# Optimization experiments

Measured on AMD Instinct MI355X. Metric: run time of the kernel, lower is better.

The kernel has to match this reference:

```python
import jax, jax.numpy as jnp
import numpy as np

N_NODES = 50000
N_EDGES = 800000
HIDDEN = 128
UNIFIED = 128


def _sage_conv(x, src, dst, W_l, b_l, W_r, n_nodes):
    # PyG SAGEConv (mean aggr): out = lin_l(mean_{j in N(i)} x_j) + lin_r(x_i)
    msgs = x[src]  # [E, d] gather of source-node features
    agg = jax.ops.segment_sum(msgs, dst, num_segments=n_nodes)  # [N, d]
    cnt = jax.ops.segment_sum(jnp.ones((src.shape[0],), dtype=x.dtype), dst,
                              num_segments=n_nodes)
    agg = agg / jnp.maximum(cnt, 1.0)[:, None]  # mean; isolated nodes -> 0
    return agg @ W_l.T + b_l + x @ W_r.T


def setup_inputs() -> dict:
    key = jax.random.key(0)
    ks = jax.random.split(key, 8)
    s = 1.0 / np.sqrt(HIDDEN)
    x = jax.random.normal(ks[0], (N_NODES, HIDDEN), dtype=jnp.float32)
    edge_index = jax.random.randint(ks[1], (2, N_EDGES), 0, N_NODES, dtype=jnp.int64)
    W1_l = jax.random.normal(ks[2], (HIDDEN, HIDDEN), dtype=jnp.float32) * s
    b1_l = jnp.zeros((HIDDEN,), dtype=jnp.float32)
    W1_r = jax.random.normal(ks[3], (HIDDEN, HIDDEN), dtype=jnp.float32) * s
    W2_l = jax.random.normal(ks[4], (UNIFIED, HIDDEN), dtype=jnp.float32) * s
    b2_l = jnp.zeros((UNIFIED,), dtype=jnp.float32)
    W2_r = jax.random.normal(ks[5], (UNIFIED, HIDDEN), dtype=jnp.float32) * s
    return {"x": x, "edge_index": edge_index,
            "W1_l": W1_l, "b1_l": b1_l, "W1_r": W1_r,
            "W2_l": W2_l, "b2_l": b2_l, "W2_r": W2_r}


def reference(x, edge_index, W1_l, b1_l, W1_r, W2_l, b2_l, W2_r):
    src, dst = edge_index[0], edge_index[1]
    n = x.shape[0]
    h = jax.nn.relu(_sage_conv(x, src, dst, W1_l, b1_l, W1_r, n))
    return _sage_conv(h, src, dst, W2_l, b2_l, W2_r, n)
```

## Files before the change

kernel.cpp:

```cpp
#include <hip/hip_runtime.h>

#define N_NODES 50000
#define HIDDEN 128
#define NBUCK ((N_NODES + 127) >> 7)
#define BCAP 2304

typedef __attribute__((ext_vector_type(8))) short short8;
typedef __attribute__((ext_vector_type(4))) float f32x4;

__device__ __forceinline__ unsigned short f2bf(float f) {
    union { float f; unsigned int u; } a; a.f = f;
    unsigned int u = a.u;
    u += 0x7FFFu + ((u >> 16) & 1u);
    return (unsigned short)(u >> 16);
}
__device__ __forceinline__ float bf2f(unsigned int bits16) {
    union { unsigned int u; float f; } a; a.u = bits16 << 16;
    return a.f;
}

__global__ __launch_bounds__(256) void pack_both(
    const float* __restrict__ W1l, const float* __restrict__ W1r,
    const float* __restrict__ W2l, const float* __restrict__ W2r,
    unsigned short* __restrict__ Wp1, unsigned short* __restrict__ Wp2,
    int* __restrict__ bcur) {
    int tid = blockIdx.x * blockDim.x + threadIdx.x;
    if (tid < NBUCK) bcur[tid] = tid * BCAP;
    const int which = tid >> 15;
    const int t2 = tid & 32767;
    int j = t2 & 7, lane = (t2 >> 3) & 63, nf = (t2 >> 9) & 7, ks = t2 >> 12;
    int k = ks * 32 + ((lane >> 4) * 8) + j;
    int t = nf * 16 + (lane & 15);
    const float* Wl = which ? W2l : W1l;
    const float* Wr = which ? W2r : W1r;
    float v = (k < 128) ? Wl[t * 128 + k] : Wr[t * 128 + (k - 128)];
    (which ? Wp2 : Wp1)[t2] = f2bf(v);
}

__global__ void cast_bf16(const float* __restrict__ x, unsigned short* __restrict__ xb, int n4) {
    int i = blockIdx.x * blockDim.x + threadIdx.x;
    if (i >= n4) return;
    float4 v = reinterpret_cast<const float4*>(x)[i];
    ushort4 o = make_ushort4(f2bf(v.x), f2bf(v.y), f2bf(v.z), f2bf(v.w));
    reinterpret_cast<ushort4*>(xb)[i] = o;
}

#define PCHUNK 4096
__global__ __launch_bounds__(1024) void partition_edges(
    const int* __restrict__ src, const int* __restrict__ dst, int E,
    int* __restrict__ bcur, unsigned int* __restrict__ packed) {
    __shared__ int h[NBUCK];
    __shared__ int base[NBUCK];
    const int tid = threadIdx.x;
    const int c0 = blockIdx.x * PCHUNK;
    for (int i = tid; i < NBUCK; i += 1024) h[i] = 0;
    __syncthreads();

    unsigned int val[4];
    int bk[4];
#pragma unroll
    for (int u = 0; u < 4; ++u) {
        const int e = c0 + u * 1024 + tid;
        if (e < E) {
            const int d = dst[e];
            val[u] = ((unsigned int)d << 16) | (unsigned int)src[e];
            bk[u] = d >> 7;
            atomicAdd(&h[bk[u]], 1);
        } else {
            bk[u] = -1;
        }
    }
    __syncthreads();
    for (int i = tid; i < NBUCK; i += 1024) {
        base[i] = h[i] ? atomicAdd(&bcur[i], h[i]) : 0;
        h[i] = 0;
    }
    __syncthreads();
#pragma unroll
    for (int u = 0; u < 4; ++u) {
        if (bk[u] >= 0) {
            const int pos = base[bk[u]] + atomicAdd(&h[bk[u]], 1);
            packed[pos] = val[u];
        }
    }
}

__global__ __launch_bounds__(256) void build_rows(const unsigned int* __restrict__ packed,
                                                  const int* __restrict__ bcur,
                                                  int* __restrict__ row_start,
                                                  int* __restrict__ row_end,
                                                  unsigned short* __restrict__ ssrc) {
    __shared__ int lh[128];
    __shared__ int lc[128];
    __shared__ int htot;
    const int b = blockIdx.x;
    const int gbase = b * BCAP, gend = bcur[b];
    const int tid = threadIdx.x;
    if (tid < 128) lh[tid] = 0;
    __syncthreads();
    for (int i = gbase + tid; i < gend; i += 256)
        atomicAdd(&lh[(packed[i] >> 16) & 127], 1);
    __syncthreads();
    int v = 0, incl = 0;
    if (tid < 128) {
        const int lane = tid & 63;
        v = lh[tid];
        incl = v;
#pragma unroll
        for (int off = 1; off < 64; off <<= 1) {
            int t = __shfl_up(incl, off);
            if (lane >= off) incl += t;
        }
        if (tid == 63) htot = incl;
    }
    __syncthreads();
    if (tid < 128) {
        const int excl = incl - v + ((tid >= 64) ? htot : 0);
        lc[tid] = gbase + excl;
        const int node = b * 128 + tid;
        if (node < N_NODES) {
            row_start[node] = gbase + excl;
            row_end[node]   = gbase + excl + v;
        }
    }
    __syncthreads();
    for (int i = gbase + tid; i < gend; i += 256) {
        const unsigned int p = packed[i];
        const int pos = atomicAdd(&lc[(p >> 16) & 127], 1);
        ssrc[pos] = (unsigned short)(p & 0xffffu);
    }
}

__global__ __launch_bounds__(256) void aggregate_mean_bf16(
    const unsigned short* __restrict__ featb, const int* __restrict__ row_start,
    const int* __restrict__ row_end, const unsigned short* __restrict__ ssrc,
    unsigned short* __restrict__ aggb) {
    const int node = blockIdx.x * 16 + (threadIdx.x >> 4);
    const int lq = threadIdx.x & 15;
    if (node >= N_NODES) return;
    const int beg = row_start[node], end = row_end[node];
    float acc[4][8];
#pragma unroll
    for (int u = 0; u < 4; ++u)
#pragma unroll
        for (int f = 0; f < 8; ++f) acc[u][f] = 0.f;

    int j = beg;
    for (; j + 3 < end; j += 4) {
#pragma unroll
        for (int u = 0; u < 4; ++u) {
            const int s = ssrc[j + u];
            const short8 v = *reinterpret_cast<const short8*>(&featb[(size_t)s * HIDDEN + 8 * lq]);
#pragma unroll
            for (int f = 0; f < 8; ++f) acc[u][f] += bf2f((unsigned short)v[f]);
        }
    }
    for (; j < end; ++j) {
        const int s = ssrc[j];
        const short8 v = *reinterpret_cast<const short8*>(&featb[(size_t)s * HIDDEN + 8 * lq]);
#pragma unroll
        for (int f = 0; f < 8; ++f) acc[0][f] += bf2f((unsigned short)v[f]);
    }
    const int d = end - beg;
    const float inv = d ? 1.0f / (float)d : 0.0f;
    short8 o;
#pragma unroll
    for (int f = 0; f < 8; ++f)
        o[f] = (short)f2bf((acc[0][f] + acc[1][f] + acc[2][f] + acc[3][f]) * inv);
    *reinterpret_cast<short8*>(&aggb[(size_t)node * HIDDEN + 8 * lq]) = o;
}

template <int WRITE_BF16_RELU>
__global__ __launch_bounds__(256) void mfma_linear(
    const unsigned short* aggb, const unsigned short* xb,
    const unsigned short* __restrict__ Wp, const float* __restrict__ bias,
    unsigned short* out_b, float* out_f) {
    const int lane = threadIdx.x & 63;
    const int wave = threadIdx.x >> 6;
    const int wm = wave >> 1, wn = wave & 1;
    const int rowbase = blockIdx.x * 64 + wm * 32;
    const int colbase = wn * 64;
    const int l15 = lane & 15, l4 = lane >> 4;

    f32x4 acc[2][4];
#pragma unroll
    for (int m = 0; m < 2; ++m)
#pragma unroll
        for (int nf = 0; nf < 4; ++nf) acc[m][nf] = (f32x4){0.f, 0.f, 0.f, 0.f};

#pragma unroll
    for (int ks = 0; ks < 8; ++ks) {
        const unsigned short* Asrc = (ks < 4) ? aggb : xb;
        const int koff = (ks & 3) * 32 + l4 * 8;
        short8 a[2];
#pragma unroll
        for (int m = 0; m < 2; ++m) {
            int row = rowbase + m * 16 + l15;
            if (row >= N_NODES) row = N_NODES - 1;
            a[m] = *reinterpret_cast<const short8*>(&Asrc[(size_t)row * HIDDEN + koff]);
        }
#pragma unroll
        for (int nf = 0; nf < 4; ++nf) {
            const int nfg = (colbase >> 4) + nf;
            short8 b = *reinterpret_cast<const short8*>(&Wp[(((size_t)ks * 8 + nfg) * 64 + lane) * 8]);
            acc[0][nf] = __builtin_amdgcn_mfma_f32_16x16x32_bf16(a[0], b, acc[0][nf], 0, 0, 0);
            acc[1][nf] = __builtin_amdgcn_mfma_f32_16x16x32_bf16(a[1], b, acc[1][nf], 0, 0, 0);
        }
    }

#pragma unroll
    for (int nf = 0; nf < 4; ++nf) {
        const int col = colbase + nf * 16 + l15;
        const float bv = bias[col];
#pragma unroll
        for (int m = 0; m < 2; ++m) {
#pragma unroll
            for (int r = 0; r < 4; ++r) {
                const int row = rowbase + m * 16 + l4 * 4 + r;
                if (row < N_NODES) {
                    float v = acc[m][nf][r] + bv;
                    if (WRITE_BF16_RELU) {
                        v = fmaxf(v, 0.0f);
                        out_b[(size_t)row * HIDDEN + col] = f2bf(v);
                    } else {
                        out_f[(size_t)row * HIDDEN + col] = v;
                    }
                }
            }
        }
    }
}

extern "C" void kernel_launch(void* const* d_in, const int* in_sizes, int n_in,
                              void* d_out, int out_size, void* d_ws, size_t ws_size,
                              hipStream_t stream) {
    const float* x   = (const float*)d_in[0];
    const int*   ei  = (const int*)d_in[1];
    const float* W1l = (const float*)d_in[2];
    const float* b1  = (const float*)d_in[3];
    const float* W1r = (const float*)d_in[4];
    const float* W2l = (const float*)d_in[5];
    const float* b2  = (const float*)d_in[6];
    const float* W2r = (const float*)d_in[7];

    const int E = in_sizes[1] / 2;
    const int* src = ei;
    const int* dst = ei + E;

    int* iws        = (int*)d_ws;
    int* bcur       = iws;
    int* row_start  = iws + 400;
    int* row_end    = iws + 50400;
    unsigned int* packed = (unsigned int*)(iws + 100400);
    unsigned short* ssrc = (unsigned short*)(iws + 100400 + NBUCK * BCAP);
    unsigned short* xb   = ssrc + (size_t)NBUCK * BCAP;
    unsigned short* aggb = xb + (size_t)N_NODES * HIDDEN;
    unsigned short* Wp1  = aggb + (size_t)N_NODES * HIDDEN;
    unsigned short* Wp2  = Wp1 + 256 * HIDDEN;

    pack_both<<<256, 256, 0, stream>>>(W1l, W1r, W2l, W2r, Wp1, Wp2, bcur);
    cast_bf16<<<(N_NODES * HIDDEN / 4 + 255) / 256, 256, 0, stream>>>(x, xb, N_NODES * HIDDEN / 4);

    partition_edges<<<(E + PCHUNK - 1) / PCHUNK, 1024, 0, stream>>>(src, dst, E, bcur, packed);
    build_rows<<<NBUCK, 256, 0, stream>>>(packed, bcur, row_start, row_end, ssrc);

    const int aggGrid = (N_NODES + 15) / 16;
    const int linGrid = (N_NODES + 63) / 64;

    aggregate_mean_bf16<<<aggGrid, 256, 0, stream>>>(xb, row_start, row_end, ssrc, aggb);
    mfma_linear<1><<<linGrid, 256, 0, stream>>>(aggb, xb, Wp1, b1, xb, nullptr);

    aggregate_mean_bf16<<<aggGrid, 256, 0, stream>>>(xb, row_start, row_end, ssrc, aggb);
    mfma_linear<0><<<linGrid, 256, 0, stream>>>(aggb, xb, Wp2, b2, nullptr, (float*)d_out);
}
```

Baseline: 146.0 us.

## Fuse cast into prep kernel, batch gather loads, retune partition and build_rows

```diff
diff --git a/kernel.cpp b/kernel.cpp
--- a/kernel.cpp
+++ b/kernel.cpp
@@ -4,6 +4,7 @@
 #define HIDDEN 128
 #define NBUCK ((N_NODES + 127) >> 7)
 #define BCAP 2304
+#define CAST_BLOCKS 6250
 
 typedef __attribute__((ext_vector_type(8))) short short8;
 typedef __attribute__((ext_vector_type(4))) float f32x4;
@@ -19,12 +20,21 @@
     return a.f;
 }
 
-__global__ __launch_bounds__(256) void pack_both(
+__global__ __launch_bounds__(256) void prep(
+    const float* __restrict__ x, unsigned short* __restrict__ xb,
     const float* __restrict__ W1l, const float* __restrict__ W1r,
     const float* __restrict__ W2l, const float* __restrict__ W2r,
     unsigned short* __restrict__ Wp1, unsigned short* __restrict__ Wp2,
     int* __restrict__ bcur) {
-    int tid = blockIdx.x * blockDim.x + threadIdx.x;
+    const int b = blockIdx.x;
+    if (b < CAST_BLOCKS) {
+        const int i = b * 256 + threadIdx.x;
+        float4 v = reinterpret_cast<const float4*>(x)[i];
+        ushort4 o = make_ushort4(f2bf(v.x), f2bf(v.y), f2bf(v.z), f2bf(v.w));
+        reinterpret_cast<ushort4*>(xb)[i] = o;
+        return;
+    }
+    const int tid = (b - CAST_BLOCKS) * 256 + threadIdx.x;
     if (tid < NBUCK) bcur[tid] = tid * BCAP;
     const int which = tid >> 15;
     const int t2 = tid & 32767;
@@ -37,15 +47,7 @@
     (which ? Wp2 : Wp1)[t2] = f2bf(v);
 }
 
-__global__ void cast_bf16(const float* __restrict__ x, unsigned short* __restrict__ xb, int n4) {
-    int i = blockIdx.x * blockDim.x + threadIdx.x;
-    if (i >= n4) return;
-    float4 v = reinterpret_cast<const float4*>(x)[i];
-    ushort4 o = make_ushort4(f2bf(v.x), f2bf(v.y), f2bf(v.z), f2bf(v.w));
-    reinterpret_cast<ushort4*>(xb)[i] = o;
-}
-
-#define PCHUNK 4096
+#define PCHUNK 2048
 __global__ __launch_bounds__(1024) void partition_edges(
     const int* __restrict__ src, const int* __restrict__ dst, int E,
     int* __restrict__ bcur, unsigned int* __restrict__ packed) {
@@ -56,10 +58,10 @@
     for (int i = tid; i < NBUCK; i += 1024) h[i] = 0;
     __syncthreads();
 
-    unsigned int val[4];
-    int bk[4];
-#pragma unroll
-    for (int u = 0; u < 4; ++u) {
+    unsigned int val[2];
+    int bk[2];
+#pragma unroll
+    for (int u = 0; u < 2; ++u) {
         const int e = c0 + u * 1024 + tid;
         if (e < E) {
             const int d = dst[e];
@@ -77,7 +79,7 @@
     }
     __syncthreads();
 #pragma unroll
-    for (int u = 0; u < 4; ++u) {
+    for (int u = 0; u < 2; ++u) {
         if (bk[u] >= 0) {
             const int pos = base[bk[u]] + atomicAdd(&h[bk[u]], 1);
             packed[pos] = val[u];
@@ -85,7 +87,7 @@
     }
 }
 
-__global__ __launch_bounds__(256) void build_rows(const unsigned int* __restrict__ packed,
+__global__ __launch_bounds__(512) void build_rows(const unsigned int* __restrict__ packed,
                                                   const int* __restrict__ bcur,
                                                   int* __restrict__ row_start,
                                                   int* __restrict__ row_end,
@@ -98,7 +100,7 @@
     const int tid = threadIdx.x;
     if (tid < 128) lh[tid] = 0;
     __syncthreads();
-    for (int i = gbase + tid; i < gend; i += 256)
+    for (int i = gbase + tid; i < gend; i += 512)
         atomicAdd(&lh[(packed[i] >> 16) & 127], 1);
     __syncthreads();
     int v = 0, incl = 0;
@@ -124,7 +126,7 @@
         }
     }
     __syncthreads();
-    for (int i = gbase + tid; i < gend; i += 256) {
+    for (int i = gbase + tid; i < gend; i += 512) {
         const unsigned int p = packed[i];
         const int pos = atomicAdd(&lc[(p >> 16) & 127], 1);
         ssrc[pos] = (unsigned short)(p & 0xffffu);
@@ -139,34 +141,51 @@
     const int lq = threadIdx.x & 15;
     if (node >= N_NODES) return;
     const int beg = row_start[node], end = row_end[node];
-    float acc[4][8];
-#pragma unroll
-    for (int u = 0; u < 4; ++u)
-#pragma unroll
-        for (int f = 0; f < 8; ++f) acc[u][f] = 0.f;
+    float acc0[8], acc1[8];
+#pragma unroll
+    for (int f = 0; f < 8; ++f) { acc0[f] = 0.f; acc1[f] = 0.f; }
 
     int j = beg;
-    for (; j + 3 < end; j += 4) {
+    for (; j + 7 < end; j += 8) {
+        short8 v[8];
+#pragma unroll
+        for (int u = 0; u < 8; ++u) {
+            const int s = ssrc[j + u];
+            v[u] = *reinterpret_cast<const short8*>(&featb[(size_t)s * HIDDEN + 8 * lq]);
+        }
+#pragma unroll
+        for (int u = 0; u < 8; ++u) {
+            float* a = (u & 1) ? acc1 : acc0;
+#pragma unroll
+            for (int f = 0; f < 8; ++f) a[f] += bf2f((unsigned short)v[u][f]);
+        }
+    }
+    if (j + 3 < end) {
+        short8 v[4];
 #pragma unroll
         for (int u = 0; u < 4; ++u) {
             const int s = ssrc[j + u];
-            const short8 v = *reinterpret_cast<const short8*>(&featb[(size_t)s * HIDDEN + 8 * lq]);
-#pragma unroll
-            for (int f = 0; f < 8; ++f) acc[u][f] += bf2f((unsigned short)v[f]);
-        }
+            v[u] = *reinterpret_cast<const short8*>(&featb[(size_t)s * HIDDEN + 8 * lq]);
+        }
+#pragma unroll
+        for (int u = 0; u < 4; ++u) {
+            float* a = (u & 1) ? acc1 : acc0;
+#pragma unroll
+            for (int f = 0; f < 8; ++f) a[f] += bf2f((unsigned short)v[u][f]);
+        }
+        j += 4;
     }
     for (; j < end; ++j) {
         const int s = ssrc[j];
         const short8 v = *reinterpret_cast<const short8*>(&featb[(size_t)s * HIDDEN + 8 * lq]);
 #pragma unroll
-        for (int f = 0; f < 8; ++f) acc[0][f] += bf2f((unsigned short)v[f]);
+        for (int f = 0; f < 8; ++f) acc0[f] += bf2f((unsigned short)v[f]);
     }
     const int d = end - beg;
     const float inv = d ? 1.0f / (float)d : 0.0f;
     short8 o;
 #pragma unroll
-    for (int f = 0; f < 8; ++f)
-        o[f] = (short)f2bf((acc[0][f] + acc[1][f] + acc[2][f] + acc[3][f]) * inv);
+    for (int f = 0; f < 8; ++f) o[f] = (short)f2bf((acc0[f] + acc1[f]) * inv);
     *reinterpret_cast<short8*>(&aggb[(size_t)node * HIDDEN + 8 * lq]) = o;
 }
 
@@ -258,11 +277,10 @@
     unsigned short* Wp1  = aggb + (size_t)N_NODES * HIDDEN;
     unsigned short* Wp2  = Wp1 + 256 * HIDDEN;
 
-    pack_both<<<256, 256, 0, stream>>>(W1l, W1r, W2l, W2r, Wp1, Wp2, bcur);
-    cast_bf16<<<(N_NODES * HIDDEN / 4 + 255) / 256, 256, 0, stream>>>(x, xb, N_NODES * HIDDEN / 4);
+    prep<<<CAST_BLOCKS + 256, 256, 0, stream>>>(x, xb, W1l, W1r, W2l, W2r, Wp1, Wp2, bcur);
 
     partition_edges<<<(E + PCHUNK - 1) / PCHUNK, 1024, 0, stream>>>(src, dst, E, bcur, packed);
-    build_rows<<<NBUCK, 256, 0, stream>>>(packed, bcur, row_start, row_end, ssrc);
+    build_rows<<<NBUCK, 512, 0, stream>>>(packed, bcur, row_start, row_end, ssrc);
 
     const int aggGrid = (N_NODES + 15) / 16;
     const int linGrid = (N_NODES + 63) / 64;
```

Result: faster. 141.3 us (-3.2%).
